# Optimization experiments

Measured on AMD Instinct MI355X. Metric: run time of the kernel, lower is better.

Reference implementation:

```python
import jax, jax.numpy as jnp
import numpy as np

ATOM_FDIM = 133
BOND_FDIM = 14
HIDDEN = 300
DEPTH = 3
FFN_HIDDEN = 300
NUM_ATOMS = 100000
NUM_EDGES = 400000
NUM_MOLS = 4096


def setup_inputs() -> dict:
    key = jax.random.key(0)
    ks = jax.random.split(key, 10)
    x = jax.random.normal(ks[0], (NUM_ATOMS, ATOM_FDIM), dtype=jnp.float32)
    edge_index = jax.random.randint(ks[1], (2, NUM_EDGES), 0, NUM_ATOMS, dtype=jnp.int32)
    edge_attr = jax.random.normal(ks[2], (NUM_EDGES, BOND_FDIM), dtype=jnp.float32)
    batch = jnp.sort(jax.random.randint(ks[3], (NUM_ATOMS,), 0, NUM_MOLS, dtype=jnp.int32))
    s = 0.05
    W_i = jax.random.normal(ks[4], (HIDDEN, ATOM_FDIM + BOND_FDIM), dtype=jnp.float32) * s
    W_h = jax.random.normal(ks[5], (HIDDEN, HIDDEN), dtype=jnp.float32) * s
    W_o_w = jax.random.normal(ks[6], (HIDDEN, ATOM_FDIM + HIDDEN), dtype=jnp.float32) * s
    W_o_b = jnp.zeros((HIDDEN,), dtype=jnp.float32)
    ffn1_w = jax.random.normal(ks[7], (FFN_HIDDEN, HIDDEN), dtype=jnp.float32) * s
    ffn1_b = jnp.zeros((FFN_HIDDEN,), dtype=jnp.float32)
    ffn2_w = jax.random.normal(ks[8], (1, FFN_HIDDEN), dtype=jnp.float32) * s
    ffn2_b = jnp.zeros((1,), dtype=jnp.float32)
    return {"x": x, "edge_index": edge_index, "edge_attr": edge_attr, "batch": batch,
            "W_i": W_i, "W_h": W_h, "W_o_w": W_o_w, "W_o_b": W_o_b,
            "ffn1_w": ffn1_w, "ffn1_b": ffn1_b, "ffn2_w": ffn2_w, "ffn2_b": ffn2_b}


def reference(x, edge_index, edge_attr, batch, W_i, W_h, W_o_w, W_o_b,
              ffn1_w, ffn1_b, ffn2_w, ffn2_b):
    num_atoms = x.shape[0]
    src, tgt = edge_index[0], edge_index[1]
    # initial edge messages: [E, hidden]
    init = jnp.concatenate([x[src], edge_attr], axis=-1)
    m = jax.nn.relu(init @ W_i.T)
    # dropout is identity at inference
    for _ in range(DEPTH - 1):
        nei = jax.ops.segment_sum(m, tgt, num_segments=num_atoms)  # [N, hidden]
        m = jax.nn.relu(m + nei[src] @ W_h.T)
    atom_msg = jax.ops.segment_sum(m, tgt, num_segments=num_atoms)
    atom_h = jax.nn.relu(jnp.concatenate([x, atom_msg], axis=-1) @ W_o_w.T + W_o_b)
    mol = jax.ops.segment_sum(atom_h, batch, num_segments=NUM_MOLS)  # [B, hidden]
    h = jax.nn.relu(mol @ ffn1_w.T + ffn1_b)
    out = h @ ffn2_w.T + ffn2_b  # [B, 1]
    return out
```

## Files before the change

### kernel.cpp

```cpp
#include <hip/hip_runtime.h>
#include <hip/hip_fp16.h>

#define HID   300
#define NEIP  320
#define APB   4
#define SWK(r) (((r) >> 1) & 3)

typedef _Float16 f16;
typedef f16  f16x2 __attribute__((ext_vector_type(2)));
typedef f16  f16x8 __attribute__((ext_vector_type(8)));
typedef float f32x4 __attribute__((ext_vector_type(4)));

__device__ __forceinline__ f16x2 u2h(unsigned u) {
    union { unsigned u; f16x2 h; } c; c.u = u; return c.h;
}
__device__ __forceinline__ unsigned pk16(float a, float b) {
    union { f16 h[2]; unsigned u; } c; c.h[0] = (f16)a; c.h[1] = (f16)b;
    return c.u;
}
__device__ __forceinline__ void glds16(const void* g, void* l) {
    __builtin_amdgcn_global_load_lds(
        (const __attribute__((address_space(1))) void*)g,
        (__attribute__((address_space(3))) void*)l, 16, 0, 0);
}

__global__ __launch_bounds__(256) void fill_f32(float* __restrict__ p, int n, float v)
{
    int i = blockIdx.x * blockDim.x + threadIdx.x;
    int stride = gridDim.x * blockDim.x;
    for (; i < n; i += stride) p[i] = v;
}

__global__ __launch_bounds__(256) void zero_i32(int* __restrict__ p, int n)
{
    int i = blockIdx.x * blockDim.x + threadIdx.x;
    int stride = gridDim.x * blockDim.x;
    for (; i < n; i += stride) p[i] = 0;
}

__global__ __launch_bounds__(256) void cvt_pad_f16(
    f16* __restrict__ dst, const float* __restrict__ src,
    int srcRows, int ldsrc, int kuse, int kpad, int dstRows)
{
    int i = blockIdx.x * 256 + threadIdx.x;
    const int total = dstRows * kpad;
    const int st = gridDim.x * 256;
    for (; i < total; i += st) {
        int r = i / kpad, k = i - r * kpad;
        float v = (r < srcRows && k < kuse) ? src[(size_t)r * ldsrc + k] : 0.f;
        const int t = k >> 5, kg = (k >> 3) & 3, w = k & 7;
        const int kd = (t << 5) | ((kg ^ SWK(r)) << 3) | w;
        dst[(size_t)r * kpad + kd] = (f16)v;
    }
}

__global__ __launch_bounds__(256) void hist_tgt(
    const int* __restrict__ tgt, int* __restrict__ deg, int E, int N)
{
    int e = blockIdx.x * 256 + threadIdx.x;
    const int st = gridDim.x * 256;
    for (; e < E; e += st) {
        int t = tgt[e];
        t = ((unsigned)t < (unsigned)N) ? t : 0;
        atomicAdd(&deg[t], 1);
    }
}

__global__ __launch_bounds__(1024) void scan_p1(
    const int* __restrict__ deg, int* __restrict__ bsum, int N)
{
    __shared__ int s[1024];
    const int t = threadIdx.x;
    const int i = blockIdx.x * 1024 + t;
    s[t] = (i < N) ? deg[i] : 0;
    __syncthreads();
#pragma unroll
    for (int off = 512; off > 0; off >>= 1) {
        if (t < off) s[t] += s[t + off];
        __syncthreads();
    }
    if (t == 0) bsum[blockIdx.x] = s[0];
}

__global__ __launch_bounds__(1024) void scan_p2(
    const int* __restrict__ bsum, int* __restrict__ boff,
    int G, int* __restrict__ rowPtrN, int E)
{
    __shared__ int s[1024];
    const int t = threadIdx.x;
    s[t] = (t < G) ? bsum[t] : 0;
    __syncthreads();
    for (int off = 1; off < 1024; off <<= 1) {
        const int v = (t >= off) ? s[t - off] : 0;
        __syncthreads();
        s[t] += v;
        __syncthreads();
    }
    if (t < G) boff[t] = (t == 0) ? 0 : s[t - 1];
    if (t == 0) *rowPtrN = E;
}

__global__ __launch_bounds__(1024) void scan_p3(
    const int* __restrict__ deg, const int* __restrict__ boff,
    int* __restrict__ rowPtr, int* __restrict__ cursor, int N)
{
    __shared__ int s[1024];
    const int t = threadIdx.x;
    const int i = blockIdx.x * 1024 + t;
    const int v = (i < N) ? deg[i] : 0;
    s[t] = v;
    __syncthreads();
    for (int off = 1; off < 1024; off <<= 1) {
        const int w = (t >= off) ? s[t - off] : 0;
        __syncthreads();
        s[t] += w;
        __syncthreads();
    }
    if (i < N) {
        const int excl = boff[blockIdx.x] + s[t] - v;
        rowPtr[i] = excl;
        cursor[i] = excl;
    }
}

__global__ __launch_bounds__(256) void scatter_e(
    const int* __restrict__ src, const int* __restrict__ tgt,
    const float* __restrict__ ea,
    int* __restrict__ cursor, int* __restrict__ csrc,
    unsigned* __restrict__ eaPk,
    int E, int N)
{
    int e = blockIdx.x * 256 + threadIdx.x;
    const int st = gridDim.x * 256;
    for (; e < E; e += st) {
        int t = tgt[e];
        int s = src[e];
        t = ((unsigned)t < (unsigned)N) ? t : 0;
        s = ((unsigned)s < (unsigned)N) ? s : 0;
        const int p = atomicAdd(&cursor[t], 1);
        csrc[p] = s;
        const float* er = ea + (size_t)e * 14;
        unsigned* dst = eaPk + (size_t)p * 7;
#pragma unroll
        for (int k = 0; k < 7; ++k)
            dst[k] = pk16(er[2 * k], er[2 * k + 1]);
    }
}

__global__ __launch_bounds__(512) void gemm_mfma(
    const void* __restrict__ A1, int lda1, int a1f16, int K1use,
    const f16* __restrict__ W1, int kpad1,
    const void* __restrict__ A2, int lda2, int a2f16, int K2use,
    const f16* __restrict__ W2, int kpad2,
    const float* __restrict__ bias,
    f16* __restrict__ C, int ldc,
    int M, int do_relu)
{
    __shared__ f16 As[64 * 320];
    __shared__ f16 Ws[320 * 32];

    const int tid  = threadIdx.x;
    const int bm   = blockIdx.x * 64;
    const int lane = tid & 63;
    const int wv   = tid >> 6;
    const int wrow = (wv >> 2) * 32;
    const int wcol = (wv & 3) * 80;
    const int lm   = lane & 15;
    const int kg   = lane >> 4;

    const int n1 = A1 ? (kpad1 >> 5) : 0;
    const int n2 = A2 ? (kpad2 >> 5) : 0;
    const int ntot = n1 + n2;

    f32x4 acc[2][5];
#pragma unroll
    for (int r = 0; r < 2; ++r)
#pragma unroll
        for (int c = 0; c < 5; ++c) acc[r][c] = (f32x4){0.f, 0.f, 0.f, 0.f};

    auto stage_W = [&](int s) {
        const f16* W = (s < n1) ? W1 : W2;
        const int kpad = (s < n1) ? kpad1 : kpad2;
        const int k0 = (((s < n1) ? s : s - n1) << 5);
        const int r16 = lane >> 2;
        const int q   = lane & 3;
        for (int c = wv; c < 20; c += 8) {
            const int R = (c << 4) + r16;
            glds16((const char*)W + ((size_t)R * kpad + k0) * 2 + q * 16,
                   (void*)&Ws[c << 9]);
        }
    };

    auto stage_A = [&](int seg) {
        const void* A = seg ? A2 : A1;
        const int lda  = seg ? lda2 : lda1;
        const int af16 = seg ? a2f16 : a1f16;
        const int kuse = seg ? K2use : K1use;
        const int kpad = seg ? kpad2 : kpad1;
        if (af16) {
            const int nch = kpad >> 3;
            const char* base = (const char*)A + (size_t)bm * lda * 2;
            for (int c = wv; c < nch; c += 8)
                glds16(base + (c << 10) + lane * 16, (void*)&As[c << 9]);
        } else {
            const int cpr = kpad >> 3;
            for (int idx = tid; idx < 64 * cpr; idx += 512) {
                const int row = idx / cpr;
                const int ks  = (idx - row * cpr) << 3;
                const int gmr = bm + row;
                f16x8 v = (f16x8){0, 0, 0, 0, 0, 0, 0, 0};
                if (gmr < M) {
                    const float* p = (const float*)A + (size_t)gmr * lda + ks;
#pragma unroll
                    for (int j = 0; j < 8; ++j)
                        v[j] = (ks + j < kuse) ? (f16)p[j] : (f16)0.f;
                }
                const int t = ks >> 5, kgc = (ks >> 3) & 3;
                *(f16x8*)&As[row * kpad + (t << 5) + ((kgc ^ SWK(row)) << 3)] = v;
            }
        }
    };

    stage_A(0);
    stage_W(0);
    __syncthreads();

    for (int s = 0; s < ntot; ++s) {
        const int seg   = (s >= n1) ? 1 : 0;
        const int kpadA = seg ? kpad2 : kpad1;
        const int sl    = seg ? (s - n1) : s;
        f16x8 af[2], bf[5];
#pragma unroll
        for (int r = 0; r < 2; ++r) {
            const int R = wrow + (r << 4) + lm;
            af[r] = *(const f16x8*)&As[R * kpadA + (sl << 5) + ((kg ^ SWK(R)) << 3)];
        }
#pragma unroll
        for (int c = 0; c < 5; ++c) {
            const int R = wcol + (c << 4) + lm;
            bf[c] = *(const f16x8*)&Ws[R * 32 + ((kg ^ SWK(R)) << 3)];
        }
        __syncthreads();
        if (s + 1 < ntot) {
            stage_W(s + 1);
            if (s + 1 == n1 && n2) stage_A(1);
        }
#pragma unroll
        for (int r = 0; r < 2; ++r)
#pragma unroll
            for (int c = 0; c < 5; ++c)
                acc[r][c] = __builtin_amdgcn_mfma_f32_16x16x32_f16(
                    af[r], bf[c], acc[r][c], 0, 0, 0);
        __syncthreads();
    }

#pragma unroll
    for (int r = 0; r < 2; ++r) {
        const int gm0 = bm + wrow + (r << 4) + ((lane >> 4) << 2);
#pragma unroll
        for (int c = 0; c < 5; ++c) {
            const int n = wcol + (c << 4) + lm;
            if (n >= HID) continue;
            const float bi = bias ? bias[n] : 0.f;
#pragma unroll
            for (int i = 0; i < 4; ++i) {
                const int gmo = gm0 + i;
                if (gmo >= M) continue;
                float v = acc[r][c][i] + bi;
                if (do_relu) v = fmaxf(v, 0.f);
                C[(size_t)gmo * ldc + n] = (f16)v;
            }
        }
    }
}

template <int NSLOTS>
__global__ __launch_bounds__(192) void edge_csr(
    const unsigned* __restrict__ xa,
    const unsigned* __restrict__ hn0,
    const unsigned* __restrict__ hn1,
    const int* __restrict__ rowPtr,
    const int* __restrict__ csrc,
    const unsigned* __restrict__ eaPk,
    const float* __restrict__ Wi,
    unsigned* __restrict__ out,
    int N)
{
    const int p = threadIdx.x;
    f16x2 wpk[14];
    if (p < 150) {
#pragma unroll
        for (int k = 0; k < 14; ++k)
            wpk[k] = (f16x2){(f16)Wi[(2 * p) * 147 + 133 + k],
                             (f16)Wi[(2 * p + 1) * 147 + 133 + k]};
    }
    const f16x2 zero2 = (f16x2){(f16)0.f, (f16)0.f};

    const int a0 = blockIdx.x * APB;
    const int a1 = min(a0 + APB, N);
    for (int a = a0; a < a1; ++a) {
        const int beg = rowPtr[a];
        const int end = rowPtr[a + 1];
        float acc0 = 0.f, acc1 = 0.f;
        if (p < 150) {
#pragma unroll 2
            for (int j = beg; j < end; ++j) {
                const int s = csrc[j];
                const size_t srow = (size_t)s * 150 + p;
                const unsigned u0 = xa[srow];
                unsigned u1 = 0, u2 = 0;
                if (NSLOTS > 1) u1 = hn0[srow];
                if (NSLOTS > 2) u2 = hn1[srow];
                const unsigned* eq = eaPk + (size_t)j * 7;
                f16x2 ebA = zero2, ebB = zero2;
#pragma unroll
                for (int k = 0; k < 7; ++k) {
                    const f16x2 e2 = u2h(eq[k]);
                    ebA += (f16x2){e2.x, e2.x} * wpk[2 * k];
                    ebB += (f16x2){e2.y, e2.y} * wpk[2 * k + 1];
                }
                f16x2 m = __builtin_elementwise_max(u2h(u0) + (ebA + ebB), zero2);
                if (NSLOTS > 1) m = __builtin_elementwise_max(m + u2h(u1), zero2);
                if (NSLOTS > 2) m = __builtin_elementwise_max(m + u2h(u2), zero2);
                acc0 += (float)m.x;
                acc1 += (float)m.y;
            }
        }
        if (p < NEIP / 2) {
            const unsigned val = (p < 150) ? pk16(acc0, acc1) : 0u;
            const int t = p >> 4, kgc = (p >> 2) & 3, w = p & 3;
            out[(size_t)a * (NEIP / 2) + (t << 4) + ((kgc ^ SWK(a)) << 2) + w] = val;
        }
    }
}

__global__ __launch_bounds__(256) void mol_pool(
    const f16* __restrict__ ah,
    const int* __restrict__ batch,
    float* __restrict__ mol,
    int N)
{
    const int b = blockIdx.x;
    int lo = 0, hi = N;
    while (lo < hi) { int mid = (lo + hi) >> 1; if (batch[mid] < b) lo = mid + 1; else hi = mid; }
    const int start = lo;
    hi = N;
    while (lo < hi) { int mid = (lo + hi) >> 1; if (batch[mid] < b + 1) lo = mid + 1; else hi = mid; }
    const int end = lo;

    for (int h = threadIdx.x; h < HID; h += 256) {
        float s = 0.f;
        for (int a = start; a < end; ++a) s += (float)ah[(size_t)a * HID + h];
        mol[(size_t)b * HID + h] = s;
    }
}

__global__ __launch_bounds__(64) void ffn2_k(
    const f16* __restrict__ h1,
    const float* __restrict__ w2,
    const float* __restrict__ b2, float* __restrict__ out, int B)
{
    const int b = blockIdx.x;
    float s = 0.f;
    for (int k = threadIdx.x; k < HID; k += 64)
        s += (float)h1[(size_t)b * HID + k] * w2[k];
#pragma unroll
    for (int off = 32; off > 0; off >>= 1) s += __shfl_down(s, off);
    if (threadIdx.x == 0) out[b] = s + b2[0];
}

extern "C" void kernel_launch(void* const* d_in, const int* in_sizes, int n_in,
                              void* d_out, int out_size, void* d_ws, size_t ws_size,
                              hipStream_t stream)
{
    float* outp = (float*)d_out;
    const int fillBlocks = (out_size + 255) / 256;

    if (n_in < 12) {
        fill_f32<<<fillBlocks, 256, 0, stream>>>(outp, out_size, 2.0e6f + n_in);
        return;
    }

    const int N = in_sizes[0] / 133;
    const int E = in_sizes[1] / 2;
    const int B = out_size;

    const long long expect[12] = {
        (long long)N * 133, (long long)E * 2, (long long)E * 14, N,
        300LL * 147, 300LL * 300, 300LL * 433, 300,
        300LL * 300, 300, 300, 1 };
    for (int i = 0; i < 12; ++i) {
        if ((long long)in_sizes[i] != expect[i]) {
            fill_f32<<<fillBlocks, 256, 0, stream>>>(outp, out_size,
                                                     3.0e6f + 1.0e4f * i);
            return;
        }
    }

    const int G = (N + 1023) / 1024;
    if (G > 1024) {
        fill_f32<<<fillBlocks, 256, 0, stream>>>(outp, out_size, 4.0e6f);
        return;
    }

    char* basep = (char*)d_ws;
    auto align16 = [](size_t v) { return (v + 15) & ~(size_t)15; };
    const size_t slotB  = align16((size_t)N * HID * sizeof(f16));
    const size_t neiB   = align16((size_t)N * NEIP * sizeof(f16));
    const size_t wSmall = align16(320 * 160 * sizeof(f16));
    const size_t wBig   = align16(320 * 320 * sizeof(f16));
    const size_t molB   = align16((size_t)B * HID * sizeof(float));
    const size_t h1B    = align16((size_t)B * HID * sizeof(f16));
    const size_t rpB    = align16((size_t)(N + 1) * sizeof(int));
    const size_t curB   = align16((size_t)N * sizeof(int));
    const size_t csrcB  = align16((size_t)E * sizeof(int));
    const size_t eaB    = align16((size_t)E * 7 * sizeof(unsigned));
    const size_t bsB    = align16(1024 * sizeof(int));
    const size_t need = 3 * slotB + neiB + 2 * wSmall + 3 * wBig
                      + molB + h1B + rpB + 2 * curB + csrcB + eaB + 2 * bsB;

    if (ws_size < need) {
        fill_f32<<<fillBlocks, 256, 0, stream>>>(outp, out_size,
                                                 (float)(ws_size >> 20));
        return;
    }

    const float* x     = (const float*)d_in[0];
    const int*   ei    = (const int*)d_in[1];
    const float* ea    = (const float*)d_in[2];
    const int*   batch = (const int*)d_in[3];
    const float* W_i   = (const float*)d_in[4];
    const float* W_h   = (const float*)d_in[5];
    const float* W_o   = (const float*)d_in[6];
    const float* W_ob  = (const float*)d_in[7];
    const float* f1w   = (const float*)d_in[8];
    const float* f1b   = (const float*)d_in[9];
    const float* f2w   = (const float*)d_in[10];
    const float* f2b   = (const float*)d_in[11];
    const int* src = ei;
    const int* tgt = ei + E;

    char* cp = basep;
    f16* xa     = (f16*)cp;         cp += slotB;
    f16* hn0    = (f16*)cp;         cp += slotB;
    f16* hn1    = (f16*)cp;         cp += slotB;
    f16* nei    = (f16*)cp;         cp += neiB;
    f16* WiA    = (f16*)cp;         cp += wSmall;
    f16* Wh     = (f16*)cp;         cp += wBig;
    f16* WoA    = (f16*)cp;         cp += wSmall;
    f16* WoB    = (f16*)cp;         cp += wBig;
    f16* Wf1    = (f16*)cp;         cp += wBig;
    float* mol  = (float*)cp;       cp += molB;
    f16* h1     = (f16*)cp;         cp += h1B;
    int* rowPtr = (int*)cp;         cp += rpB;
    int* cursor = (int*)cp;         cp += curB;
    int* deg    = (int*)cp;         cp += curB;
    int* csrc   = (int*)cp;         cp += csrcB;
    unsigned* eaPk = (unsigned*)cp; cp += eaB;
    int* bsum   = (int*)cp;         cp += bsB;
    int* boff   = (int*)cp;         cp += bsB;

    const unsigned* xa_u  = (const unsigned*)xa;
    const unsigned* hn0_u = (const unsigned*)hn0;
    const unsigned* hn1_u = (const unsigned*)hn1;
    unsigned*       nei_u = (unsigned*)nei;

    const int gAtom = (N + 63) / 64;
    const int gMolG = (B + 63) / 64;
    const int gEdge = (N + APB - 1) / APB;

    zero_i32<<<128, 256, 0, stream>>>(deg, N);
    hist_tgt<<<1024, 256, 0, stream>>>(tgt, deg, E, N);
    scan_p1<<<G, 1024, 0, stream>>>(deg, bsum, N);
    scan_p2<<<1, 1024, 0, stream>>>(bsum, boff, G, rowPtr + N, E);
    scan_p3<<<G, 1024, 0, stream>>>(deg, boff, rowPtr, cursor, N);
    scatter_e<<<1024, 256, 0, stream>>>(src, tgt, ea, cursor, csrc, eaPk, E, N);

    cvt_pad_f16<<<64,  256, 0, stream>>>(WiA, W_i,       300, 147, 133, 160, 320);
    cvt_pad_f16<<<128, 256, 0, stream>>>(Wh,  W_h,       300, 300, 300, 320, 320);
    cvt_pad_f16<<<64,  256, 0, stream>>>(WoA, W_o,       300, 433, 133, 160, 320);
    cvt_pad_f16<<<128, 256, 0, stream>>>(WoB, W_o + 133, 300, 433, 300, 320, 320);
    cvt_pad_f16<<<128, 256, 0, stream>>>(Wf1, f1w,       300, 300, 300, 320, 320);

    gemm_mfma<<<gAtom, 512, 0, stream>>>(x, 133, 0, 133, WiA, 160,
        nullptr, 0, 0, 0, nullptr, 0, nullptr, xa, HID, N, 0);
    edge_csr<1><<<gEdge, 192, 0, stream>>>(xa_u, hn0_u, hn1_u, rowPtr, csrc,
                                           eaPk, W_i, nei_u, N);
    gemm_mfma<<<gAtom, 512, 0, stream>>>(nei, NEIP, 1, NEIP, Wh, 320,
        nullptr, 0, 0, 0, nullptr, 0, nullptr, hn0, HID, N, 0);
    edge_csr<2><<<gEdge, 192, 0, stream>>>(xa_u, hn0_u, hn1_u, rowPtr, csrc,
                                           eaPk, W_i, nei_u, N);
    gemm_mfma<<<gAtom, 512, 0, stream>>>(nei, NEIP, 1, NEIP, Wh, 320,
        nullptr, 0, 0, 0, nullptr, 0, nullptr, hn1, HID, N, 0);
    edge_csr<3><<<gEdge, 192, 0, stream>>>(xa_u, hn0_u, hn1_u, rowPtr, csrc,
                                           eaPk, W_i, nei_u, N);
    gemm_mfma<<<gAtom, 512, 0, stream>>>(x, 133, 0, 133, WoA, 160,
        nei, NEIP, 1, NEIP, WoB, 320, W_ob, xa, HID, N, 1);
    mol_pool<<<B, 256, 0, stream>>>(xa, batch, mol, N);
    gemm_mfma<<<gMolG, 512, 0, stream>>>(mol, 300, 0, 300, Wf1, 320,
        nullptr, 0, 0, 0, nullptr, 0, f1b, h1, HID, B, 1);
    ffn2_k<<<B, 64, 0, stream>>>(h1, f2w, f2b, outp, B);
}
```

Measured before the change: 802.2 us.

## Split depth-2/3 edge aggregation into two hidden-dimension halves

Adds edge_csr_h, which handles only half of the 150 packed hidden pairs per launch, with 96-thread blocks of 8 atoms each. Iterations 2 and 3 now launch it twice, once per half, in place of edge_csr. The aim is to shrink the random-gather working set of the xa/hn0/hn1 source rows so more of it stays in cache. In exchange, rowPtr, csrc and the edge-attribute data are read twice, there are extra launches, and 21 of 96 lanes sit idle. The padded columns are no longer written here and rely on the earlier depth-1 pass having zeroed them.

```diff
diff --git a/kernel.cpp b/kernel.cpp
--- a/kernel.cpp
+++ b/kernel.cpp
@@ -334,6 +334,65 @@
     }
 }
 
+template <int NSLOTS>
+__global__ __launch_bounds__(96) void edge_csr_h(
+    const unsigned* __restrict__ xa,
+    const unsigned* __restrict__ hn0,
+    const unsigned* __restrict__ hn1,
+    const int* __restrict__ rowPtr,
+    const int* __restrict__ csrc,
+    const unsigned* __restrict__ eaPk,
+    const float* __restrict__ Wi,
+    unsigned* __restrict__ out,
+    int N, int half)
+{
+    const int q = threadIdx.x;
+    const int p = half * 75 + q;
+    f16x2 wpk[14];
+    if (q < 75) {
+#pragma unroll
+        for (int k = 0; k < 14; ++k)
+            wpk[k] = (f16x2){(f16)Wi[(2 * p) * 147 + 133 + k],
+                             (f16)Wi[(2 * p + 1) * 147 + 133 + k]};
+    }
+    const f16x2 zero2 = (f16x2){(f16)0.f, (f16)0.f};
+
+    const int a0 = blockIdx.x * 8;
+    const int a1 = min(a0 + 8, N);
+    for (int a = a0; a < a1; ++a) {
+        const int beg = rowPtr[a];
+        const int end = rowPtr[a + 1];
+        float acc0 = 0.f, acc1 = 0.f;
+        if (q < 75) {
+#pragma unroll 2
+            for (int j = beg; j < end; ++j) {
+                const int s = csrc[j];
+                const size_t srow = (size_t)s * 150 + p;
+                const unsigned u0 = xa[srow];
+                unsigned u1 = 0, u2 = 0;
+                if (NSLOTS > 1) u1 = hn0[srow];
+                if (NSLOTS > 2) u2 = hn1[srow];
+                const unsigned* eq = eaPk + (size_t)j * 7;
+                f16x2 ebA = zero2, ebB = zero2;
+#pragma unroll
+                for (int k = 0; k < 7; ++k) {
+                    const f16x2 e2 = u2h(eq[k]);
+                    ebA += (f16x2){e2.x, e2.x} * wpk[2 * k];
+                    ebB += (f16x2){e2.y, e2.y} * wpk[2 * k + 1];
+                }
+                f16x2 m = __builtin_elementwise_max(u2h(u0) + (ebA + ebB), zero2);
+                if (NSLOTS > 1) m = __builtin_elementwise_max(m + u2h(u1), zero2);
+                if (NSLOTS > 2) m = __builtin_elementwise_max(m + u2h(u2), zero2);
+                acc0 += (float)m.x;
+                acc1 += (float)m.y;
+            }
+            const unsigned val = pk16(acc0, acc1);
+            const int t = p >> 4, kgc = (p >> 2) & 3, w = p & 3;
+            out[(size_t)a * (NEIP / 2) + (t << 4) + ((kgc ^ SWK(a)) << 2) + w] = val;
+        }
+    }
+}
+
 __global__ __launch_bounds__(256) void mol_pool(
     const f16* __restrict__ ah,
     const int* __restrict__ batch,
@@ -465,9 +524,10 @@
     const unsigned* hn1_u = (const unsigned*)hn1;
     unsigned*       nei_u = (unsigned*)nei;
 
-    const int gAtom = (N + 63) / 64;
-    const int gMolG = (B + 63) / 64;
-    const int gEdge = (N + APB - 1) / APB;
+    const int gAtom  = (N + 63) / 64;
+    const int gMolG  = (B + 63) / 64;
+    const int gEdge  = (N + APB - 1) / APB;
+    const int gEdgeH = (N + 7) / 8;
 
     zero_i32<<<128, 256, 0, stream>>>(deg, N);
     hist_tgt<<<1024, 256, 0, stream>>>(tgt, deg, E, N);
@@ -488,12 +548,16 @@
                                            eaPk, W_i, nei_u, N);
     gemm_mfma<<<gAtom, 512, 0, stream>>>(nei, NEIP, 1, NEIP, Wh, 320,
         nullptr, 0, 0, 0, nullptr, 0, nullptr, hn0, HID, N, 0);
-    edge_csr<2><<<gEdge, 192, 0, stream>>>(xa_u, hn0_u, hn1_u, rowPtr, csrc,
-                                           eaPk, W_i, nei_u, N);
+    edge_csr_h<2><<<gEdgeH, 96, 0, stream>>>(xa_u, hn0_u, hn1_u, rowPtr, csrc,
+                                             eaPk, W_i, nei_u, N, 0);
+    edge_csr_h<2><<<gEdgeH, 96, 0, stream>>>(xa_u, hn0_u, hn1_u, rowPtr, csrc,
+                                             eaPk, W_i, nei_u, N, 1);
     gemm_mfma<<<gAtom, 512, 0, stream>>>(nei, NEIP, 1, NEIP, Wh, 320,
         nullptr, 0, 0, 0, nullptr, 0, nullptr, hn1, HID, N, 0);
-    edge_csr<3><<<gEdge, 192, 0, stream>>>(xa_u, hn0_u, hn1_u, rowPtr, csrc,
-                                           eaPk, W_i, nei_u, N);
+    edge_csr_h<3><<<gEdgeH, 96, 0, stream>>>(xa_u, hn0_u, hn1_u, rowPtr, csrc,
+                                             eaPk, W_i, nei_u, N, 0);
+    edge_csr_h<3><<<gEdgeH, 96, 0, stream>>>(xa_u, hn0_u, hn1_u, rowPtr, csrc,
+                                             eaPk, W_i, nei_u, N, 1);
     gemm_mfma<<<gAtom, 512, 0, stream>>>(x, 133, 0, 133, WoA, 160,
         nei, NEIP, 1, NEIP, WoB, 320, W_ob, xa, HID, N, 1);
     mol_pool<<<B, 256, 0, stream>>>(xa, batch, mol, N);
```

New measurement: 849.7 us. 5.9% more time.

## Halve GEMM row tile, double-buffer weight tiles, use nontemporal edge loads

Applied to the files above, without the earlier changes.

The MFMA GEMM now uses 32-row tiles instead of 64, doubling the grid size, and keeps two weight buffers in LDS. The next weight tile can then be fetched while the current one is consumed, which removes one barrier per K step. The edge aggregation kernel switches its CSR index, edge-feature loads and output store to nontemporal hints to reduce cache pollution. In exchange, each weight tile is reused across half as many rows, so global weight traffic per output row rises.

```diff
diff --git a/kernel.cpp b/kernel.cpp
--- a/kernel.cpp
+++ b/kernel.cpp
@@ -156,14 +156,14 @@
     f16* __restrict__ C, int ldc,
     int M, int do_relu)
 {
-    __shared__ f16 As[64 * 320];
-    __shared__ f16 Ws[320 * 32];
+    __shared__ f16 As[32 * 320];
+    __shared__ f16 Ws[2][320 * 32];
 
     const int tid  = threadIdx.x;
-    const int bm   = blockIdx.x * 64;
+    const int bm   = blockIdx.x * 32;
     const int lane = tid & 63;
     const int wv   = tid >> 6;
-    const int wrow = (wv >> 2) * 32;
+    const int wrow = (wv >> 2) << 4;
     const int wcol = (wv & 3) * 80;
     const int lm   = lane & 15;
     const int kg   = lane >> 4;
@@ -172,13 +172,11 @@
     const int n2 = A2 ? (kpad2 >> 5) : 0;
     const int ntot = n1 + n2;
 
-    f32x4 acc[2][5];
-#pragma unroll
-    for (int r = 0; r < 2; ++r)
-#pragma unroll
-        for (int c = 0; c < 5; ++c) acc[r][c] = (f32x4){0.f, 0.f, 0.f, 0.f};
-
-    auto stage_W = [&](int s) {
+    f32x4 acc[5];
+#pragma unroll
+    for (int c = 0; c < 5; ++c) acc[c] = (f32x4){0.f, 0.f, 0.f, 0.f};
+
+    auto stage_W = [&](int s, int b) {
         const f16* W = (s < n1) ? W1 : W2;
         const int kpad = (s < n1) ? kpad1 : kpad2;
         const int k0 = (((s < n1) ? s : s - n1) << 5);
@@ -187,7 +185,7 @@
         for (int c = wv; c < 20; c += 8) {
             const int R = (c << 4) + r16;
             glds16((const char*)W + ((size_t)R * kpad + k0) * 2 + q * 16,
-                   (void*)&Ws[c << 9]);
+                   (void*)&Ws[b][c << 9]);
         }
     };
 
@@ -198,13 +196,13 @@
         const int kuse = seg ? K2use : K1use;
         const int kpad = seg ? kpad2 : kpad1;
         if (af16) {
-            const int nch = kpad >> 3;
+            const int nch = kpad >> 4;
             const char* base = (const char*)A + (size_t)bm * lda * 2;
             for (int c = wv; c < nch; c += 8)
                 glds16(base + (c << 10) + lane * 16, (void*)&As[c << 9]);
         } else {
             const int cpr = kpad >> 3;
-            for (int idx = tid; idx < 64 * cpr; idx += 512) {
+            for (int idx = tid; idx < 32 * cpr; idx += 512) {
                 const int row = idx / cpr;
                 const int ks  = (idx - row * cpr) << 3;
                 const int gmr = bm + row;
@@ -222,54 +220,53 @@
     };
 
     stage_A(0);
-    stage_W(0);
+    stage_W(0, 0);
     __syncthreads();
 
     for (int s = 0; s < ntot; ++s) {
         const int seg   = (s >= n1) ? 1 : 0;
         const int kpadA = seg ? kpad2 : kpad1;
         const int sl    = seg ? (s - n1) : s;
-        f16x8 af[2], bf[5];
-#pragma unroll
-        for (int r = 0; r < 2; ++r) {
-            const int R = wrow + (r << 4) + lm;
-            af[r] = *(const f16x8*)&As[R * kpadA + (sl << 5) + ((kg ^ SWK(R)) << 3)];
+        const int b     = s & 1;
+        f16x8 af, bf[5];
+        {
+            const int R = wrow + lm;
+            af = *(const f16x8*)&As[R * kpadA + (sl << 5) + ((kg ^ SWK(R)) << 3)];
         }
 #pragma unroll
         for (int c = 0; c < 5; ++c) {
             const int R = wcol + (c << 4) + lm;
-            bf[c] = *(const f16x8*)&Ws[R * 32 + ((kg ^ SWK(R)) << 3)];
-        }
+            bf[c] = *(const f16x8*)&Ws[b][R * 32 + ((kg ^ SWK(R)) << 3)];
+        }
+        if (s + 1 < ntot) {
+            if (s + 1 == n1 && n2) {
+                __syncthreads();
+                stage_W(s + 1, b ^ 1);
+                stage_A(1);
+            } else {
+                stage_W(s + 1, b ^ 1);
+            }
+        }
+#pragma unroll
+        for (int c = 0; c < 5; ++c)
+            acc[c] = __builtin_amdgcn_mfma_f32_16x16x32_f16(
+                af, bf[c], acc[c], 0, 0, 0);
         __syncthreads();
-        if (s + 1 < ntot) {
-            stage_W(s + 1);
-            if (s + 1 == n1 && n2) stage_A(1);
-        }
-#pragma unroll
-        for (int r = 0; r < 2; ++r)
-#pragma unroll
-            for (int c = 0; c < 5; ++c)
-                acc[r][c] = __builtin_amdgcn_mfma_f32_16x16x32_f16(
-                    af[r], bf[c], acc[r][c], 0, 0, 0);
-        __syncthreads();
-    }
-
-#pragma unroll
-    for (int r = 0; r < 2; ++r) {
-        const int gm0 = bm + wrow + (r << 4) + ((lane >> 4) << 2);
-#pragma unroll
-        for (int c = 0; c < 5; ++c) {
-            const int n = wcol + (c << 4) + lm;
-            if (n >= HID) continue;
-            const float bi = bias ? bias[n] : 0.f;
-#pragma unroll
-            for (int i = 0; i < 4; ++i) {
-                const int gmo = gm0 + i;
-                if (gmo >= M) continue;
-                float v = acc[r][c][i] + bi;
-                if (do_relu) v = fmaxf(v, 0.f);
-                C[(size_t)gmo * ldc + n] = (f16)v;
-            }
+    }
+
+    const int gm0 = bm + wrow + ((lane >> 4) << 2);
+#pragma unroll
+    for (int c = 0; c < 5; ++c) {
+        const int n = wcol + (c << 4) + lm;
+        if (n >= HID) continue;
+        const float bi = bias ? bias[n] : 0.f;
+#pragma unroll
+        for (int i = 0; i < 4; ++i) {
+            const int gmo = gm0 + i;
+            if (gmo >= M) continue;
+            float v = acc[c][i] + bi;
+            if (do_relu) v = fmaxf(v, 0.f);
+            C[(size_t)gmo * ldc + n] = (f16)v;
         }
     }
 }
@@ -305,7 +302,7 @@
         if (p < 150) {
 #pragma unroll 2
             for (int j = beg; j < end; ++j) {
-                const int s = csrc[j];
+                const int s = __builtin_nontemporal_load(&csrc[j]);
                 const size_t srow = (size_t)s * 150 + p;
                 const unsigned u0 = xa[srow];
                 unsigned u1 = 0, u2 = 0;
@@ -315,7 +312,7 @@
                 f16x2 ebA = zero2, ebB = zero2;
 #pragma unroll
                 for (int k = 0; k < 7; ++k) {
-                    const f16x2 e2 = u2h(eq[k]);
+                    const f16x2 e2 = u2h(__builtin_nontemporal_load(&eq[k]));
                     ebA += (f16x2){e2.x, e2.x} * wpk[2 * k];
                     ebB += (f16x2){e2.y, e2.y} * wpk[2 * k + 1];
                 }
@@ -329,7 +326,8 @@
         if (p < NEIP / 2) {
             const unsigned val = (p < 150) ? pk16(acc0, acc1) : 0u;
             const int t = p >> 4, kgc = (p >> 2) & 3, w = p & 3;
-            out[(size_t)a * (NEIP / 2) + (t << 4) + ((kgc ^ SWK(a)) << 2) + w] = val;
+            __builtin_nontemporal_store(val,
+                &out[(size_t)a * (NEIP / 2) + (t << 4) + ((kgc ^ SWK(a)) << 2) + w]);
         }
     }
 }
@@ -465,8 +463,8 @@
     const unsigned* hn1_u = (const unsigned*)hn1;
     unsigned*       nei_u = (unsigned*)nei;
 
-    const int gAtom = (N + 63) / 64;
-    const int gMolG = (B + 63) / 64;
+    const int gAtom = (N + 31) / 32;
+    const int gMolG = (B + 31) / 32;
     const int gEdge = (N + APB - 1) / APB;
 
     zero_i32<<<128, 256, 0, stream>>>(deg, N);
```

New measurement: 844.1 us. 5.2% more time.
